# Performance work log

Measured on AMD Instinct MI355X. Metric: run time of the kernel, lower is better.

Reference implementation:

```python
import jax, jax.numpy as jnp
import numpy as np

N_NODES = 50000
N_EDGES = 600000
D = 128
ITERATIONS = 3


def setup_inputs() -> dict:
    key = jax.random.key(0)
    k0, k1, k2, k3 = jax.random.split(key, 4)
    node_feats = jax.random.normal(k0, (N_NODES, D), dtype=jnp.float32)
    adjacency = jax.random.randint(k1, (N_EDGES, 2), 0, N_NODES, dtype=jnp.int64)
    scale = 1.0 / np.sqrt(D).astype(np.float32)
    W_emb = jax.random.normal(k2, (D, D), dtype=jnp.float32) * scale
    b_emb = jnp.zeros((D,), dtype=jnp.float32)
    W_upd = jax.random.normal(k3, (D, D), dtype=jnp.float32) * scale
    b_upd = jnp.zeros((D,), dtype=jnp.float32)
    return {
        "node_feats": node_feats,
        "W_emb": W_emb,
        "b_emb": b_emb,
        "W_upd": W_upd,
        "b_upd": b_upd,
        "adjacency": adjacency,
    }


def reference(node_feats, W_emb, b_emb, W_upd, b_upd, adjacency):
    # Embedding layer: Dense + ReLU per node (inference path skips BatchNorm)
    h = jax.nn.relu(node_feats @ W_emb + b_emb)  # [N, D]

    src = adjacency[:, 0]
    dst = adjacency[:, 1]

    # Each undirected edge contributes a message in both directions.
    ones = jnp.ones((N_EDGES,), dtype=h.dtype)
    deg = (jax.ops.segment_sum(ones, src, num_segments=N_NODES)
           + jax.ops.segment_sum(ones, dst, num_segments=N_NODES))  # [N]
    denom = (deg + 1.0)[:, None]  # +1 for the node's own contribution

    for _ in range(ITERATIONS):
        # MessagePassing: gather neighbor features, scatter-add into nodes,
        # then normalize by (num incoming messages + 1).
        agg = (jax.ops.segment_sum(h[dst], src, num_segments=N_NODES)
               + jax.ops.segment_sum(h[src], dst, num_segments=N_NODES))  # [N, D]
        h = (h + agg) / denom
        # Update: per-node Dense followed by sigmoid nonlinearity.
        h = jax.nn.sigmoid(h @ W_upd + b_upd)
    return h
```

## Files before the change

### kernel.cpp

```cpp
#include <hip/hip_runtime.h>
#include <hip/hip_bf16.h>

#define NN 50000
#define NE 600000
#define DD 128
#define RB 64
#define NSHARD_DIV 6250
#define GB ((NN + RB - 1) / RB)
#define EBQ ((NE + 1023) / 1024)
#define SB ((NN + 1023) / 1024)

typedef __bf16 bfrag __attribute__((ext_vector_type(8)));
typedef float  ffrag __attribute__((ext_vector_type(4)));
typedef unsigned uintv4 __attribute__((ext_vector_type(4)));
typedef unsigned uintv2 __attribute__((ext_vector_type(2)));

union frag_cast { uintv4 u4; unsigned u[4]; bfrag b; };

__device__ __forceinline__ float bfbits2f(unsigned v) { return __uint_as_float(v << 16); }
__device__ __forceinline__ unsigned f2bfbits(float f) {
    unsigned u = __float_as_uint(f);
    return (u + 0x7FFFu + ((u >> 16) & 1u)) >> 16;
}

__device__ __forceinline__ float ld_in(const void* p, int idx, int f32) {
    return f32 ? ((const float*)p)[idx]
               : bfbits2f(((const unsigned short*)p)[idx]);
}

__device__ __forceinline__ void ld_edge_nt(const int* adj, int e, int i64, int& s, int& d) {
    if (i64) {
        s = __builtin_nontemporal_load(&adj[4 * e]);
        d = __builtin_nontemporal_load(&adj[4 * e + 2]);
    } else {
        s = __builtin_nontemporal_load(&adj[2 * e]);
        d = __builtin_nontemporal_load(&adj[2 * e + 1]);
    }
}

__global__ void k_prep(const unsigned* __restrict__ Ww, const unsigned* __restrict__ adjw,
                       const void* __restrict__ We, const void* __restrict__ Wu,
                       unsigned short* __restrict__ WeT, unsigned short* __restrict__ WuT,
                       int* __restrict__ flags, int* __restrict__ deg) {
    const int tid = threadIdx.x;
    if (blockIdx.x < DD) {
        __shared__ int scnt;
        if (tid == 0) scnt = 0;
        __syncthreads();
        int c = 0;
        for (int i = tid; i < 512; i += 256) {
            unsigned e = (Ww[i] >> 7) & 0xFFu;
            c += (e >= 0x60u && e <= 0x85u) ? 1 : 0;
        }
        atomicAdd(&scnt, c);
        __syncthreads();
        const int f32 = (scnt >= 256) ? 0 : 1;
        const int k = blockIdx.x;
        if (tid < DD) {
            WeT[tid * DD + k] = (unsigned short)f2bfbits(ld_in(We, k * DD + tid, f32));
        } else {
            int n = tid - DD;
            WuT[n * DD + k] = (unsigned short)f2bfbits(ld_in(Wu, k * DD + n, f32));
        }
        return;
    }
    for (int i = (blockIdx.x - DD) * 256 + tid; i < NN; i += 64 * 256) deg[i] = 0;
    if (blockIdx.x != DD) return;
    __shared__ int cnt[2];
    if (tid < 2) cnt[tid] = 0;
    __syncthreads();
    int c0 = 0, c1 = 0;
    for (int i = tid; i < 512; i += 256) {
        unsigned e = (Ww[i] >> 7) & 0xFFu;
        c0 += (e >= 0x60u && e <= 0x85u) ? 1 : 0;
        c1 += (adjw[2 * i + 1] == 0u) ? 1 : 0;
    }
    atomicAdd(&cnt[0], c0);
    atomicAdd(&cnt[1], c1);
    __syncthreads();
    if (tid == 0) {
        flags[0] = (cnt[0] >= 256) ? 0 : 1;
        flags[1] = (cnt[1] >= 256) ? 1 : 0;
    }
}

__device__ __forceinline__ void mfma_rows(const bfrag af[4], const unsigned short* sWT,
                                          int m, int quad, ffrag acc[8]) {
#pragma unroll
    for (int ks = 0; ks < 4; ks++) {
        const int k0 = ks * 32 + quad * 8;
#pragma unroll
        for (int ct = 0; ct < 8; ct++) {
            bfrag bf_ = *(const bfrag*)&sWT[(ct * 16 + m) * DD + k0];
            acc[ct] = __builtin_amdgcn_mfma_f32_16x16x32_bf16(af[ks], bf_, acc[ct], 0, 0, 0);
        }
    }
}

__launch_bounds__(256, 5)
__global__ void k_main1(const void* __restrict__ Xp, const unsigned short* __restrict__ WTg,
                        const void* __restrict__ Bp, unsigned short* __restrict__ Hout,
                        const int* __restrict__ flags, const int* __restrict__ adj,
                        int* __restrict__ deg, uintv2* __restrict__ edg) {
    __shared__ __align__(16) unsigned short sWT[DD * DD];
    const int tid = threadIdx.x;
    if (blockIdx.x >= GB) {
        const int bb = blockIdx.x - GB;
        const int i64 = flags[1];
#pragma unroll
        for (int k = 0; k < 4; k++) {
            const int e = bb * 1024 + k * 256 + tid;
            if (e < NE) {
                int s, d;
                ld_edge_nt(adj, e, i64, s, d);
                uintv2 out;
                if ((unsigned)s < NN && (unsigned)d < NN) {
                    int ks = atomicAdd(&deg[s], 1);
                    int kd = atomicAdd(&deg[d], 1);
                    out[0] = (unsigned)s | ((unsigned)d << 16);
                    out[1] = (unsigned)ks | ((unsigned)kd << 16);
                } else {
                    out[0] = 0xFFFFFFFFu;
                    out[1] = 0;
                }
                __builtin_nontemporal_store(out, &edg[e]);
            }
        }
        return;
    }
    const int wave = tid >> 6;
    const int lane = tid & 63;
    const int f32  = flags[0];
    const int m    = lane & 15;
    const int quad = lane >> 4;
    const int rowbase = blockIdx.x * RB + wave * 16;
    const int row  = rowbase + m;
    const int rc   = (row < NN) ? row : (NN - 1);

    for (int i = tid; i < 2048; i += 256)
        ((uintv4*)sWT)[i] = ((const uintv4*)WTg)[i];

    bfrag af[4];
    if (f32) {
        const float4* Xf = (const float4*)Xp;
#pragma unroll
        for (int ks = 0; ks < 4; ks++) {
            const int k0 = ks * 32 + quad * 8;
            float4 a0 = Xf[rc * 32 + (k0 >> 2)];
            float4 a1 = Xf[rc * 32 + (k0 >> 2) + 1];
            frag_cast fc;
            fc.u[0] = f2bfbits(a0.x) | (f2bfbits(a0.y) << 16);
            fc.u[1] = f2bfbits(a0.z) | (f2bfbits(a0.w) << 16);
            fc.u[2] = f2bfbits(a1.x) | (f2bfbits(a1.y) << 16);
            fc.u[3] = f2bfbits(a1.z) | (f2bfbits(a1.w) << 16);
            af[ks] = fc.b;
        }
    } else {
        const uintv4* Xv = (const uintv4*)Xp;
#pragma unroll
        for (int ks = 0; ks < 4; ks++) {
            const int k0 = ks * 32 + quad * 8;
            frag_cast fc;
            fc.u4 = Xv[rc * 16 + (k0 >> 3)];
            af[ks] = fc.b;
        }
    }
    __syncthreads();

    ffrag acc[8];
#pragma unroll
    for (int i = 0; i < 8; i++) acc[i] = (ffrag)(0.0f);
    mfma_rows(af, sWT, m, quad, acc);

#pragma unroll
    for (int ct = 0; ct < 8; ct++) {
        int col = ct * 16 + m;
        float bb = ld_in(Bp, col, f32);
#pragma unroll
        for (int reg = 0; reg < 4; reg++) {
            int orow = rowbase + quad * 4 + reg;
            if (orow < NN) {
                float z = fmaxf(acc[ct][reg] + bb, 0.0f);
                Hout[orow * DD + col] = (unsigned short)f2bfbits(z);
            }
        }
    }
}

__global__ void k_scan1(const int* __restrict__ deg, int* __restrict__ rows,
                        int* __restrict__ sums) {
    __shared__ int wsum[16];
    __shared__ int woff[16];
    const int tid  = threadIdx.x;
    const int wid  = tid >> 6;
    const int lane = tid & 63;
    const int i = blockIdx.x * 1024 + tid;
    int x = (i < NN) ? deg[i] : 0;
#pragma unroll
    for (int off = 1; off < 64; off <<= 1) {
        int y = __shfl_up(x, off, 64);
        if (lane >= off) x += y;
    }
    if (lane == 63) wsum[wid] = x;
    __syncthreads();
    if (wid == 0) {
        int s  = (lane < 16) ? wsum[lane] : 0;
        int xs = s;
#pragma unroll
        for (int off = 1; off < 16; off <<= 1) {
            int y = __shfl_up(xs, off, 64);
            if (lane >= off) xs += y;
        }
        if (lane < 16) woff[lane] = xs - s;
        if (lane == 15) sums[blockIdx.x] = xs;
    }
    __syncthreads();
    if (i < NN) rows[i + 1] = x + woff[wid];
}

__global__ void k_scan2(int* __restrict__ sums, int nb) {
    int t = threadIdx.x;
    int v = (t < nb) ? sums[t] : 0;
    int x = v;
    for (int off = 1; off < 64; off <<= 1) {
        int y = __shfl_up(x, off, 64);
        if (t >= off) x += y;
    }
    if (t < nb) sums[t] = x - v;
}

__global__ void k_scan3(const int* __restrict__ sums, int* __restrict__ rows) {
    int i = blockIdx.x * 1024 + threadIdx.x;
    if (i < NN) {
        rows[i + 1] += sums[blockIdx.x];
        if (i == 0) rows[0] = 0;
    }
}

__launch_bounds__(256)
__global__ void k_fill2(const uintv2* __restrict__ edg, const int* __restrict__ rows,
                        unsigned short* __restrict__ nbr) {
    const int shard = blockIdx.x & 7;
    const int bb = blockIdx.x >> 3;
#pragma unroll
    for (int k = 0; k < 4; k++) {
        const int e = bb * 1024 + k * 256 + threadIdx.x;
        if (e >= NE) continue;
        uintv2 v = __builtin_nontemporal_load(&edg[e]);
        if (v[0] == 0xFFFFFFFFu) continue;
        const int s = v[0] & 0xFFFFu, d = v[0] >> 16;
        if (s / NSHARD_DIV == shard) nbr[rows[s] + (v[1] & 0xFFFFu)] = (unsigned short)d;
        if (d / NSHARD_DIV == shard) nbr[rows[d] + (v[1] >> 16)]    = (unsigned short)s;
    }
}

__launch_bounds__(256)
__global__ void k_gather(const unsigned* __restrict__ H32, const int* __restrict__ rows,
                         const unsigned short* __restrict__ nbr,
                         unsigned* __restrict__ XB32) {
    const int row  = (blockIdx.x * 256 + threadIdx.x) >> 6;
    const int lane = threadIdx.x & 63;
    if (row >= NN) return;
    unsigned selfv = H32[row * 64 + lane];
    float ax = bfbits2f(selfv & 0xFFFFu);
    float ay = bfbits2f(selfv >> 16);
    const int st = rows[row], en = rows[row + 1];
    int j = st;
    for (; j + 16 <= en; j += 16) {
        int n[16];
#pragma unroll
        for (int t = 0; t < 16; t++) n[t] = __builtin_nontemporal_load(&nbr[j + t]);
        unsigned v[16];
#pragma unroll
        for (int t = 0; t < 16; t++) v[t] = H32[n[t] * 64 + lane];
#pragma unroll
        for (int t = 0; t < 16; t++) {
            ax += bfbits2f(v[t] & 0xFFFFu);
            ay += bfbits2f(v[t] >> 16);
        }
    }
    for (; j + 4 <= en; j += 4) {
        int n0 = __builtin_nontemporal_load(&nbr[j]);
        int n1 = __builtin_nontemporal_load(&nbr[j + 1]);
        int n2 = __builtin_nontemporal_load(&nbr[j + 2]);
        int n3 = __builtin_nontemporal_load(&nbr[j + 3]);
        unsigned v0 = H32[n0 * 64 + lane];
        unsigned v1 = H32[n1 * 64 + lane];
        unsigned v2 = H32[n2 * 64 + lane];
        unsigned v3 = H32[n3 * 64 + lane];
        ax += (bfbits2f(v0 & 0xFFFFu) + bfbits2f(v1 & 0xFFFFu)) +
              (bfbits2f(v2 & 0xFFFFu) + bfbits2f(v3 & 0xFFFFu));
        ay += (bfbits2f(v0 >> 16) + bfbits2f(v1 >> 16)) +
              (bfbits2f(v2 >> 16) + bfbits2f(v3 >> 16));
    }
    for (; j < en; ++j) {
        unsigned v = H32[(int)__builtin_nontemporal_load(&nbr[j]) * 64 + lane];
        ax += bfbits2f(v & 0xFFFFu);
        ay += bfbits2f(v >> 16);
    }
    float inv = 1.0f / (float)(en - st + 1);
    unsigned packed = f2bfbits(ax * inv) | (f2bfbits(ay * inv) << 16);
    __builtin_nontemporal_store(packed, &XB32[row * 64 + lane]);
}

__launch_bounds__(256, 5)
__global__ void k_gemmB(const unsigned short* __restrict__ XB,
                        const unsigned short* __restrict__ WTg, const void* __restrict__ Bp,
                        unsigned short* __restrict__ HoutBf, float* __restrict__ HoutF,
                        const int* __restrict__ flags, int last) {
    __shared__ __align__(16) unsigned short sWT[DD * DD];
    const int tid  = threadIdx.x;
    const int wave = tid >> 6;
    const int lane = tid & 63;
    const int f32  = flags[0];
    const int m    = lane & 15;
    const int quad = lane >> 4;
    const int rowbase = blockIdx.x * RB + wave * 16;
    const int row  = rowbase + m;

    for (int i = tid; i < 2048; i += 256)
        ((uintv4*)sWT)[i] = ((const uintv4*)WTg)[i];

    bfrag af[4];
    const uintv4* Xv = (const uintv4*)XB;
#pragma unroll
    for (int ks = 0; ks < 4; ks++) {
        const int k0 = ks * 32 + quad * 8;
        frag_cast fc;
        fc.u4 = __builtin_nontemporal_load(&Xv[row * 16 + (k0 >> 3)]);
        af[ks] = fc.b;
    }
    __syncthreads();

    ffrag acc[8];
#pragma unroll
    for (int i = 0; i < 8; i++) acc[i] = (ffrag)(0.0f);
    mfma_rows(af, sWT, m, quad, acc);

#pragma unroll
    for (int ct = 0; ct < 8; ct++) {
        int col = ct * 16 + m;
        float bb = ld_in(Bp, col, f32);
#pragma unroll
        for (int reg = 0; reg < 4; reg++) {
            int orow = rowbase + quad * 4 + reg;
            if (orow < NN) {
                float s = 1.0f / (1.0f + __expf(-(acc[ct][reg] + bb)));
                if (!last) {
                    HoutBf[orow * DD + col] = (unsigned short)f2bfbits(s);
                } else if (f32) {
                    HoutF[orow * DD + col] = s;
                } else {
                    ((unsigned short*)HoutF)[orow * DD + col] = (unsigned short)f2bfbits(s);
                }
            }
        }
    }
}

extern "C" void kernel_launch(void* const* d_in, const int* in_sizes, int n_in,
                              void* d_out, int out_size, void* d_ws, size_t ws_size,
                              hipStream_t stream) {
    const void* X  = d_in[0];
    const void* We = d_in[1];
    const void* be = d_in[2];
    const void* Wu = d_in[3];
    const void* bu = d_in[4];
    const int* adj = (const int*)d_in[5];

    char* p = (char*)d_ws;
    int* FLAGS = (int*)p;                       p += 256;
    int* ROWS  = (int*)p;                       p += ((NN + 1) * 4 + 252) / 256 * 256;
    int* SUMS  = (int*)p;                       p += 256;
    unsigned short* NBR = (unsigned short*)p;   p += (size_t)2 * NE * 2;
    unsigned short* WeT = (unsigned short*)p;   p += DD * DD * 2;
    unsigned short* WuT = (unsigned short*)p;   p += DD * DD * 2;
    uintv2* EDG2 = (uintv2*)p;                  p += (size_t)NE * 8;
    unsigned short* XB  = (unsigned short*)p;
    int* DEG = (int*)XB;

    unsigned short* HA = (unsigned short*)d_out + (size_t)NN * DD;

    k_prep<<<DD + 64, 256, 0, stream>>>((const unsigned*)We, (const unsigned*)adj,
                                        We, Wu, WeT, WuT, FLAGS, DEG);
    k_main1<<<GB + EBQ, 256, 0, stream>>>(X, WeT, be, HA, FLAGS, adj, DEG, EDG2);
    k_scan1<<<SB, 1024, 0, stream>>>(DEG, ROWS, SUMS);
    k_scan2<<<1, 64, 0, stream>>>(SUMS, SB);
    k_scan3<<<SB, 1024, 0, stream>>>(SUMS, ROWS);
    k_fill2<<<8 * EBQ, 256, 0, stream>>>(EDG2, ROWS, NBR);

    const int GGB = (NN * 64 + 255) / 256;
    for (int it = 0; it < 3; ++it) {
        int last = (it == 2);
        k_gather<<<GGB, 256, 0, stream>>>((const unsigned*)HA, ROWS, NBR, (unsigned*)XB);
        k_gemmB<<<GB, 256, 0, stream>>>(XB, WuT, bu, HA, (float*)d_out, FLAGS, last);
    }
}
```

Measured before the change: 379.8 us.

## Fuse neighbor gather with update GEMM and widen gather to 16-byte loads

```diff
diff --git a/kernel.cpp b/kernel.cpp
--- a/kernel.cpp
+++ b/kernel.cpp
@@ -254,53 +254,116 @@
     }
 }
 
+__device__ __forceinline__ void acc8(float a[8], uintv4 v) {
+#pragma unroll
+    for (int i = 0; i < 4; i++) {
+        a[2 * i]     += bfbits2f(v[i] & 0xFFFFu);
+        a[2 * i + 1] += bfbits2f(v[i] >> 16);
+    }
+}
+
+__device__ __forceinline__ uintv4 gather_row(const uintv4* __restrict__ Hv,
+                                             const int* __restrict__ rows,
+                                             const unsigned short* __restrict__ nbr,
+                                             int rc, int cpart) {
+    const int st = rows[rc], en = rows[rc + 1];
+    uintv4 sv = Hv[rc * 16 + cpart];
+    float a[8];
+#pragma unroll
+    for (int i = 0; i < 4; i++) {
+        a[2 * i]     = bfbits2f(sv[i] & 0xFFFFu);
+        a[2 * i + 1] = bfbits2f(sv[i] >> 16);
+    }
+    int j = st;
+    for (; j + 4 <= en; j += 4) {
+        int n0 = nbr[j], n1 = nbr[j + 1], n2 = nbr[j + 2], n3 = nbr[j + 3];
+        uintv4 v0 = Hv[n0 * 16 + cpart];
+        uintv4 v1 = Hv[n1 * 16 + cpart];
+        uintv4 v2 = Hv[n2 * 16 + cpart];
+        uintv4 v3 = Hv[n3 * 16 + cpart];
+        acc8(a, v0); acc8(a, v1); acc8(a, v2); acc8(a, v3);
+    }
+    for (; j < en; ++j) acc8(a, Hv[(int)nbr[j] * 16 + cpart]);
+    const float inv = 1.0f / (float)(en - st + 1);
+    uintv4 pk;
+#pragma unroll
+    for (int i = 0; i < 4; i++)
+        pk[i] = f2bfbits(a[2 * i] * inv) | (f2bfbits(a[2 * i + 1] * inv) << 16);
+    return pk;
+}
+
+__launch_bounds__(256, 3)
+__global__ void k_iter(const unsigned short* __restrict__ Hin, const int* __restrict__ rows,
+                       const unsigned short* __restrict__ nbr,
+                       const unsigned short* __restrict__ WTg, const void* __restrict__ Bp,
+                       unsigned short* __restrict__ Hout, const int* __restrict__ flags) {
+    __shared__ __align__(16) unsigned short sWT[DD * DD];
+    __shared__ __align__(16) unsigned short sXB[4 * 16 * DD];
+    const int tid  = threadIdx.x;
+    const int wave = tid >> 6;
+    const int lane = tid & 63;
+    const int m    = lane & 15;
+    const int quad = lane >> 4;
+    const int cpart = lane & 15;
+    const int rowbase = blockIdx.x * RB + wave * 16;
+
+    for (int i = tid; i < 2048; i += 256)
+        ((uintv4*)sWT)[i] = ((const uintv4*)WTg)[i];
+
+    const uintv4* Hv = (const uintv4*)Hin;
+    for (int b = 0; b < 4; b++) {
+        const int r  = rowbase + b * 4 + quad;
+        const int rc = (r < NN) ? r : (NN - 1);
+        uintv4 pk = gather_row(Hv, rows, nbr, rc, cpart);
+        const int rr = b * 4 + quad;
+        unsigned off = (unsigned)(wave * 4096 + rr * 256 + cpart * 16);
+        off ^= (unsigned)((rr & 7) << 4);
+        *(uintv4*)((char*)sXB + off) = pk;
+    }
+    __syncthreads();
+
+    bfrag af[4];
+#pragma unroll
+    for (int ks = 0; ks < 4; ks++) {
+        unsigned off = (unsigned)(wave * 4096 + m * 256 + ks * 64 + quad * 16);
+        off ^= (unsigned)((m & 7) << 4);
+        af[ks] = *(const bfrag*)((const char*)sXB + off);
+    }
+
+    ffrag acc[8];
+#pragma unroll
+    for (int i = 0; i < 8; i++) acc[i] = (ffrag)(0.0f);
+    mfma_rows(af, sWT, m, quad, acc);
+
+    const int f32 = flags[0];
+#pragma unroll
+    for (int ct = 0; ct < 8; ct++) {
+        int col = ct * 16 + m;
+        float bb = ld_in(Bp, col, f32);
+#pragma unroll
+        for (int reg = 0; reg < 4; reg++) {
+            int orow = rowbase + quad * 4 + reg;
+            if (orow < NN) {
+                float s = 1.0f / (1.0f + __expf(-(acc[ct][reg] + bb)));
+                Hout[orow * DD + col] = (unsigned short)f2bfbits(s);
+            }
+        }
+    }
+}
+
 __launch_bounds__(256)
-__global__ void k_gather(const unsigned* __restrict__ H32, const int* __restrict__ rows,
-                         const unsigned short* __restrict__ nbr,
-                         unsigned* __restrict__ XB32) {
-    const int row  = (blockIdx.x * 256 + threadIdx.x) >> 6;
-    const int lane = threadIdx.x & 63;
-    if (row >= NN) return;
-    unsigned selfv = H32[row * 64 + lane];
-    float ax = bfbits2f(selfv & 0xFFFFu);
-    float ay = bfbits2f(selfv >> 16);
-    const int st = rows[row], en = rows[row + 1];
-    int j = st;
-    for (; j + 16 <= en; j += 16) {
-        int n[16];
-#pragma unroll
-        for (int t = 0; t < 16; t++) n[t] = __builtin_nontemporal_load(&nbr[j + t]);
-        unsigned v[16];
-#pragma unroll
-        for (int t = 0; t < 16; t++) v[t] = H32[n[t] * 64 + lane];
-#pragma unroll
-        for (int t = 0; t < 16; t++) {
-            ax += bfbits2f(v[t] & 0xFFFFu);
-            ay += bfbits2f(v[t] >> 16);
-        }
-    }
-    for (; j + 4 <= en; j += 4) {
-        int n0 = __builtin_nontemporal_load(&nbr[j]);
-        int n1 = __builtin_nontemporal_load(&nbr[j + 1]);
-        int n2 = __builtin_nontemporal_load(&nbr[j + 2]);
-        int n3 = __builtin_nontemporal_load(&nbr[j + 3]);
-        unsigned v0 = H32[n0 * 64 + lane];
-        unsigned v1 = H32[n1 * 64 + lane];
-        unsigned v2 = H32[n2 * 64 + lane];
-        unsigned v3 = H32[n3 * 64 + lane];
-        ax += (bfbits2f(v0 & 0xFFFFu) + bfbits2f(v1 & 0xFFFFu)) +
-              (bfbits2f(v2 & 0xFFFFu) + bfbits2f(v3 & 0xFFFFu));
-        ay += (bfbits2f(v0 >> 16) + bfbits2f(v1 >> 16)) +
-              (bfbits2f(v2 >> 16) + bfbits2f(v3 >> 16));
-    }
-    for (; j < en; ++j) {
-        unsigned v = H32[(int)__builtin_nontemporal_load(&nbr[j]) * 64 + lane];
-        ax += bfbits2f(v & 0xFFFFu);
-        ay += bfbits2f(v >> 16);
-    }
-    float inv = 1.0f / (float)(en - st + 1);
-    unsigned packed = f2bfbits(ax * inv) | (f2bfbits(ay * inv) << 16);
-    __builtin_nontemporal_store(packed, &XB32[row * 64 + lane]);
+__global__ void k_gath2(const unsigned short* __restrict__ Hin, const int* __restrict__ rows,
+                        const unsigned short* __restrict__ nbr, unsigned* __restrict__ XB32) {
+    const int tid  = threadIdx.x;
+    const int wave = tid >> 6;
+    const int lane = tid & 63;
+    const int quad = lane >> 4;
+    const int cpart = lane & 15;
+    const int r  = blockIdx.x * 16 + wave * 4 + quad;
+    const int rc = (r < NN) ? r : (NN - 1);
+    uintv4 pk = gather_row((const uintv4*)Hin, rows, nbr, rc, cpart);
+    if (r < NN)
+        __builtin_nontemporal_store(pk, (uintv4*)XB32 + r * 16 + cpart);
 }
 
 __launch_bounds__(256, 5)
@@ -375,9 +438,9 @@
     unsigned short* NBR = (unsigned short*)p;   p += (size_t)2 * NE * 2;
     unsigned short* WeT = (unsigned short*)p;   p += DD * DD * 2;
     unsigned short* WuT = (unsigned short*)p;   p += DD * DD * 2;
-    uintv2* EDG2 = (uintv2*)p;                  p += (size_t)NE * 8;
-    unsigned short* XB  = (unsigned short*)p;
-    int* DEG = (int*)XB;
+    unsigned short* HW  = (unsigned short*)p;
+    uintv2* EDG2 = (uintv2*)p;
+    int* DEG = (int*)(p + (size_t)NE * 8);
 
     unsigned short* HA = (unsigned short*)d_out + (size_t)NN * DD;
 
@@ -389,10 +452,10 @@
     k_scan3<<<SB, 1024, 0, stream>>>(SUMS, ROWS);
     k_fill2<<<8 * EBQ, 256, 0, stream>>>(EDG2, ROWS, NBR);
 
-    const int GGB = (NN * 64 + 255) / 256;
-    for (int it = 0; it < 3; ++it) {
-        int last = (it == 2);
-        k_gather<<<GGB, 256, 0, stream>>>((const unsigned*)HA, ROWS, NBR, (unsigned*)XB);
-        k_gemmB<<<GB, 256, 0, stream>>>(XB, WuT, bu, HA, (float*)d_out, FLAGS, last);
-    }
-}
+    k_iter<<<GB, 256, 0, stream>>>(HA, ROWS, NBR, WuT, bu, HW, FLAGS);
+    k_iter<<<GB, 256, 0, stream>>>(HW, ROWS, NBR, WuT, bu, HA, FLAGS);
+
+    const int G2B = (NN + 15) / 16;
+    k_gath2<<<G2B, 256, 0, stream>>>(HA, ROWS, NBR, (unsigned*)HW);
+    k_gemmB<<<GB, 256, 0, stream>>>(HW, WuT, bu, HA, (float*)d_out, FLAGS, 1);
+}
```

Result: slower. 403.6 us (+6.3%).

## Shard hidden features into column-blocked layout for L2-friendly neighbor gather

Applied to the files above, without the earlier changes.

```diff
diff --git a/kernel.cpp b/kernel.cpp
--- a/kernel.cpp
+++ b/kernel.cpp
@@ -9,6 +9,7 @@
 #define GB ((NN + RB - 1) / RB)
 #define EBQ ((NE + 1023) / 1024)
 #define SB ((NN + 1023) / 1024)
+#define GQB (8 * ((NN + 31) / 32))
 
 typedef __bf16 bfrag __attribute__((ext_vector_type(8)));
 typedef float  ffrag __attribute__((ext_vector_type(4)));
@@ -84,14 +85,23 @@
     }
 }
 
-__device__ __forceinline__ void mfma_rows(const bfrag af[4], const unsigned short* sWT,
+__device__ __forceinline__ void stage_w(const uintv4* __restrict__ WTg, uintv4* sW, int tid) {
+#pragma unroll
+    for (int k = 0; k < 8; k++) {
+        int i = k * 256 + tid;
+        int row = i >> 4, u = i & 15;
+        int dst = (((row >> 4) * 4 + (u >> 2)) * 4 + (u & 3)) * 16 + (row & 15);
+        sW[dst] = WTg[i];
+    }
+}
+
+__device__ __forceinline__ void mfma_rows(const bfrag af[4], const bfrag* sW,
                                           int m, int quad, ffrag acc[8]) {
 #pragma unroll
     for (int ks = 0; ks < 4; ks++) {
-        const int k0 = ks * 32 + quad * 8;
 #pragma unroll
         for (int ct = 0; ct < 8; ct++) {
-            bfrag bf_ = *(const bfrag*)&sWT[(ct * 16 + m) * DD + k0];
+            bfrag bf_ = sW[((ct * 4 + ks) * 4 + quad) * 16 + m];
             acc[ct] = __builtin_amdgcn_mfma_f32_16x16x32_bf16(af[ks], bf_, acc[ct], 0, 0, 0);
         }
     }
@@ -137,8 +147,7 @@
     const int row  = rowbase + m;
     const int rc   = (row < NN) ? row : (NN - 1);
 
-    for (int i = tid; i < 2048; i += 256)
-        ((uintv4*)sWT)[i] = ((const uintv4*)WTg)[i];
+    stage_w((const uintv4*)WTg, (uintv4*)sWT, tid);
 
     bfrag af[4];
     if (f32) {
@@ -170,7 +179,7 @@
     ffrag acc[8];
 #pragma unroll
     for (int i = 0; i < 8; i++) acc[i] = (ffrag)(0.0f);
-    mfma_rows(af, sWT, m, quad, acc);
+    mfma_rows(af, (const bfrag*)sWT, m, quad, acc);
 
 #pragma unroll
     for (int ct = 0; ct < 8; ct++) {
@@ -181,7 +190,7 @@
             int orow = rowbase + quad * 4 + reg;
             if (orow < NN) {
                 float z = fmaxf(acc[ct][reg] + bb, 0.0f);
-                Hout[orow * DD + col] = (unsigned short)f2bfbits(z);
+                Hout[ct * (NN * 16) + orow * 16 + m] = (unsigned short)f2bfbits(z);
             }
         }
     }
@@ -255,52 +264,48 @@
 }
 
 __launch_bounds__(256)
-__global__ void k_gather(const unsigned* __restrict__ H32, const int* __restrict__ rows,
-                         const unsigned short* __restrict__ nbr,
-                         unsigned* __restrict__ XB32) {
-    const int row  = (blockIdx.x * 256 + threadIdx.x) >> 6;
-    const int lane = threadIdx.x & 63;
-    if (row >= NN) return;
-    unsigned selfv = H32[row * 64 + lane];
-    float ax = bfbits2f(selfv & 0xFFFFu);
-    float ay = bfbits2f(selfv >> 16);
-    const int st = rows[row], en = rows[row + 1];
+__global__ void k_gath3(const unsigned* __restrict__ Hp, const int* __restrict__ rows,
+                        const unsigned short* __restrict__ nbr,
+                        unsigned* __restrict__ XB32) {
+    const int shard = blockIdx.x & 7;
+    const int node  = (blockIdx.x >> 3) * 32 + (threadIdx.x >> 3);
+    const int cs    = threadIdx.x & 7;
+    const int nc    = (node < NN) ? node : (NN - 1);
+    const unsigned* P = Hp + (size_t)shard * (NN * 8);
+    const int st = rows[nc], en = rows[nc + 1];
+    unsigned sv = P[nc * 8 + cs];
+    float ax = bfbits2f(sv & 0xFFFFu);
+    float ay = bfbits2f(sv >> 16);
     int j = st;
-    for (; j + 16 <= en; j += 16) {
-        int n[16];
-#pragma unroll
-        for (int t = 0; t < 16; t++) n[t] = __builtin_nontemporal_load(&nbr[j + t]);
-        unsigned v[16];
-#pragma unroll
-        for (int t = 0; t < 16; t++) v[t] = H32[n[t] * 64 + lane];
-#pragma unroll
-        for (int t = 0; t < 16; t++) {
+    for (; j + 8 <= en; j += 8) {
+        int n[8];
+#pragma unroll
+        for (int t = 0; t < 8; t++) n[t] = nbr[j + t];
+        unsigned v[8];
+#pragma unroll
+        for (int t = 0; t < 8; t++) v[t] = P[n[t] * 8 + cs];
+#pragma unroll
+        for (int t = 0; t < 8; t++) {
             ax += bfbits2f(v[t] & 0xFFFFu);
             ay += bfbits2f(v[t] >> 16);
         }
     }
-    for (; j + 4 <= en; j += 4) {
-        int n0 = __builtin_nontemporal_load(&nbr[j]);
-        int n1 = __builtin_nontemporal_load(&nbr[j + 1]);
-        int n2 = __builtin_nontemporal_load(&nbr[j + 2]);
-        int n3 = __builtin_nontemporal_load(&nbr[j + 3]);
-        unsigned v0 = H32[n0 * 64 + lane];
-        unsigned v1 = H32[n1 * 64 + lane];
-        unsigned v2 = H32[n2 * 64 + lane];
-        unsigned v3 = H32[n3 * 64 + lane];
-        ax += (bfbits2f(v0 & 0xFFFFu) + bfbits2f(v1 & 0xFFFFu)) +
-              (bfbits2f(v2 & 0xFFFFu) + bfbits2f(v3 & 0xFFFFu));
-        ay += (bfbits2f(v0 >> 16) + bfbits2f(v1 >> 16)) +
-              (bfbits2f(v2 >> 16) + bfbits2f(v3 >> 16));
+    for (; j + 2 <= en; j += 2) {
+        int n0 = nbr[j], n1 = nbr[j + 1];
+        unsigned v0 = P[n0 * 8 + cs], v1 = P[n1 * 8 + cs];
+        ax += bfbits2f(v0 & 0xFFFFu) + bfbits2f(v1 & 0xFFFFu);
+        ay += bfbits2f(v0 >> 16) + bfbits2f(v1 >> 16);
     }
     for (; j < en; ++j) {
-        unsigned v = H32[(int)__builtin_nontemporal_load(&nbr[j]) * 64 + lane];
+        unsigned v = P[(int)nbr[j] * 8 + cs];
         ax += bfbits2f(v & 0xFFFFu);
         ay += bfbits2f(v >> 16);
     }
-    float inv = 1.0f / (float)(en - st + 1);
-    unsigned packed = f2bfbits(ax * inv) | (f2bfbits(ay * inv) << 16);
-    __builtin_nontemporal_store(packed, &XB32[row * 64 + lane]);
+    const float inv = 1.0f / (float)(en - st + 1);
+    if (node < NN) {
+        unsigned pk = f2bfbits(ax * inv) | (f2bfbits(ay * inv) << 16);
+        __builtin_nontemporal_store(pk, &XB32[node * 64 + shard * 8 + cs]);
+    }
 }
 
 __launch_bounds__(256, 5)
@@ -318,8 +323,7 @@
     const int rowbase = blockIdx.x * RB + wave * 16;
     const int row  = rowbase + m;
 
-    for (int i = tid; i < 2048; i += 256)
-        ((uintv4*)sWT)[i] = ((const uintv4*)WTg)[i];
+    stage_w((const uintv4*)WTg, (uintv4*)sWT, tid);
 
     bfrag af[4];
     const uintv4* Xv = (const uintv4*)XB;
@@ -335,7 +339,7 @@
     ffrag acc[8];
 #pragma unroll
     for (int i = 0; i < 8; i++) acc[i] = (ffrag)(0.0f);
-    mfma_rows(af, sWT, m, quad, acc);
+    mfma_rows(af, (const bfrag*)sWT, m, quad, acc);
 
 #pragma unroll
     for (int ct = 0; ct < 8; ct++) {
@@ -347,7 +351,7 @@
             if (orow < NN) {
                 float s = 1.0f / (1.0f + __expf(-(acc[ct][reg] + bb)));
                 if (!last) {
-                    HoutBf[orow * DD + col] = (unsigned short)f2bfbits(s);
+                    HoutBf[ct * (NN * 16) + orow * 16 + m] = (unsigned short)f2bfbits(s);
                 } else if (f32) {
                     HoutF[orow * DD + col] = s;
                 } else {
@@ -375,9 +379,9 @@
     unsigned short* NBR = (unsigned short*)p;   p += (size_t)2 * NE * 2;
     unsigned short* WeT = (unsigned short*)p;   p += DD * DD * 2;
     unsigned short* WuT = (unsigned short*)p;   p += DD * DD * 2;
-    uintv2* EDG2 = (uintv2*)p;                  p += (size_t)NE * 8;
-    unsigned short* XB  = (unsigned short*)p;
-    int* DEG = (int*)XB;
+    unsigned short* HW  = (unsigned short*)p;
+    uintv2* EDG2 = (uintv2*)p;
+    int* DEG = (int*)(p + (size_t)NE * 8);
 
     unsigned short* HA = (unsigned short*)d_out + (size_t)NN * DD;
 
@@ -389,10 +393,9 @@
     k_scan3<<<SB, 1024, 0, stream>>>(SUMS, ROWS);
     k_fill2<<<8 * EBQ, 256, 0, stream>>>(EDG2, ROWS, NBR);
 
-    const int GGB = (NN * 64 + 255) / 256;
     for (int it = 0; it < 3; ++it) {
         int last = (it == 2);
-        k_gather<<<GGB, 256, 0, stream>>>((const unsigned*)HA, ROWS, NBR, (unsigned*)XB);
-        k_gemmB<<<GB, 256, 0, stream>>>(XB, WuT, bu, HA, (float*)d_out, FLAGS, last);
-    }
-}
+        k_gath3<<<GQB, 256, 0, stream>>>((const unsigned*)HA, ROWS, NBR, (unsigned*)HW);
+        k_gemmB<<<GB, 256, 0, stream>>>(HW, WuT, bu, HA, (float*)d_out, FLAGS, last);
+    }
+}
```

Result: no change. 381.1 us (+0.3%).
